# Kernel tuning notes

Hardware: AMD Instinct MI355X
Metric: run time of the kernel (lower is better)

Reference implementation:

```python
import jax, jax.numpy as jnp
import numpy as np
import math

B, N, D, H = 4, 2048, 1024, 16
DH = D // H  # dim per head
OUT = 1024

def setup_inputs() -> dict:
    key0 = jax.random.key(0)
    ks = jax.random.split(key0, 12)
    s = 1.0 / math.sqrt(D)
    return {
        "key": jax.random.normal(ks[0], (B, N, D), jnp.float32),
        "value": jax.random.normal(ks[1], (B, N, D), jnp.float32),
        "query": jax.random.normal(ks[2], (B, N, D), jnp.float32),
        "Wk": jax.random.normal(ks[3], (D, D), jnp.float32) * s,
        "bk": jax.random.normal(ks[4], (D,), jnp.float32) * 0.01,
        "Wv": jax.random.normal(ks[5], (D, D), jnp.float32) * s,
        "bv": jax.random.normal(ks[6], (D,), jnp.float32) * 0.01,
        "Wq": jax.random.normal(ks[7], (D, D), jnp.float32) * s,
        "bq": jax.random.normal(ks[8], (D,), jnp.float32) * 0.01,
        "Wo": jax.random.normal(ks[9], (D, OUT), jnp.float32) * s,
        "bo": jax.random.normal(ks[10], (OUT,), jnp.float32) * 0.01,
    }

def reference(key, value, query, Wk, bk, Wv, bv, Wq, bq, Wo, bo):
    scale = math.sqrt(DH)
    k = (key @ Wk + bk).reshape(B, N, H, DH).transpose(0, 2, 1, 3)    # [B,H,N,DH]
    v = (value @ Wv + bv).reshape(B, N, H, DH).transpose(0, 2, 1, 3)
    q = ((query @ Wq + bq) / scale).reshape(B, N, H, DH).transpose(0, 2, 1, 3)
    scores = jnp.einsum('bhqd,bhkd->bhqk', q, k).astype(jnp.float32)  # [B,H,N,N]
    attn = jax.nn.softmax(scores, axis=-1).astype(q.dtype)
    # dropout p=0.0 (eval / identity)
    ctx = jnp.einsum('bhqk,bhkd->bhqd', attn, v)                      # [B,H,N,DH]
    ctx = ctx.transpose(0, 2, 1, 3).reshape(B, N, D)
    out = ctx @ Wo + bo                                               # [B,N,OUT]
    return out
```

## Files before the change

kernel.cpp:

```cpp
#include <hip/hip_runtime.h>
#include <hip/hip_bf16.h>
#include <stdint.h>

#define BB 4
#define NN 2048
#define DD 1024
#define HH 16
#define DHH 64
#define MM (BB*NN)

typedef unsigned short u16;
typedef unsigned int u32;
typedef __bf16 bf16x8_t __attribute__((ext_vector_type(8)));
typedef float f32x4_t __attribute__((ext_vector_type(4)));
typedef float f32x16_t __attribute__((ext_vector_type(16)));

__device__ inline u16 f2b(float f) {
    __hip_bfloat16 h = __float2bfloat16(f);
    return *(u16*)&h;
}

__device__ inline u32 pack2(float lo, float hi) {
    __hip_bfloat162 h2 = __float22bfloat162_rn(make_float2(lo, hi));
    return *(u32*)&h2;
}

__device__ inline void gload16(const void* g, void* l) {
    __builtin_amdgcn_global_load_lds(
        (const __attribute__((address_space(1))) void*)g,
        (__attribute__((address_space(3))) void*)l, 16, 0, 0);
}

__global__ void cvt_kernel(const float* __restrict__ in, u16* __restrict__ out) {
    int i = (blockIdx.x * 256 + threadIdx.x) * 4;
    float4 v = *(const float4*)(in + i);
    ushort4 o;
    o.x = f2b(v.x); o.y = f2b(v.y); o.z = f2b(v.z); o.w = f2b(v.w);
    *(ushort4*)(out + i) = o;
}

__global__ void wtrans_kernel(const float* __restrict__ W0, const float* __restrict__ W1,
                              const float* __restrict__ W2, const float* __restrict__ W3,
                              u16* __restrict__ out_base) {
    int z = blockIdx.z;
    const float* W = (z == 0) ? W0 : (z == 1) ? W1 : (z == 2) ? W2 : W3;
    u16* o = out_base + (size_t)z * DD * DD;
    __shared__ float tile[64][65];
    int t = threadIdx.x;
    int r0 = t >> 6;
    int c = t & 63;
    int kb = blockIdx.x, nb = blockIdx.y;
#pragma unroll
    for (int i = 0; i < 16; ++i) {
        int r = i * 4 + r0;
        tile[r][c] = W[(size_t)(kb * 64 + r) * DD + nb * 64 + c];
    }
    __syncthreads();
#pragma unroll
    for (int i = 0; i < 16; ++i) {
        int r = i * 4 + r0;
        o[(size_t)(nb * 64 + r) * DD + kb * 64 + c] = f2b(tile[c][r]);
    }
}

__global__ void vtrans_kernel(const u16* __restrict__ in, u16* __restrict__ out) {
    __shared__ u16 tile[64][65];
    const int t = threadIdx.x;
    const int r0 = t >> 6;
    const int c = t & 63;
    const int nt = blockIdx.x;
    const int bh = blockIdx.y;
    const int b = bh >> 4, h = bh & 15;
    const u16* src = in + ((size_t)(b * 2048 + nt * 64)) * DD + h * 64;
#pragma unroll
    for (int i = 0; i < 16; ++i) {
        int r = i * 4 + r0;
        tile[r][c] = src[(size_t)r * DD + c];
    }
    __syncthreads();
    u16* dst = out + ((size_t)bh * 64) * NN + nt * 64;
#pragma unroll
    for (int i = 0; i < 16; ++i) {
        int r = i * 4 + r0;
        dst[(size_t)r * NN + c] = tile[c][r];
    }
}

template<int OUT_F32>
__global__ __launch_bounds__(256, 2)
void gemm_bt(const u16* __restrict__ A, const u16* __restrict__ Bt,
             const float* __restrict__ bias, void* __restrict__ Cout, float scale) {
    __shared__ u16 As[128 * 64];
    __shared__ u16 Bs[128 * 64];
    const int t = threadIdx.x;
    const int w = t >> 6, l = t & 63;
    const int wm = w >> 1, wn = w & 1;
    const int g = l >> 4, c = l & 15;
    const int bm = blockIdx.x, bn = blockIdx.y;

    const f32x4_t vzero = {0.f, 0.f, 0.f, 0.f};
    f32x4_t acc[4][4];
#pragma unroll
    for (int m = 0; m < 4; ++m)
#pragma unroll
        for (int n = 0; n < 4; ++n) acc[m][n] = vzero;

    const int srow = l >> 3;
    const int scol = ((l & 7) ^ srow) << 3;
    const int sa = (l & 7) << 4;

    for (int ks = 0; ks < 16; ++ks) {
#pragma unroll
        for (int i = 0; i < 4; ++i) {
            int chunk = w * 4 + i;
            int row = chunk * 8 + srow;
            const u16* ga = A + (size_t)(bm * 128 + row) * DD + ks * 64 + scol;
            gload16(ga, As + chunk * 512);
            const u16* gb = Bt + (size_t)(bn * 128 + row) * DD + ks * 64 + scol;
            gload16(gb, Bs + chunk * 512);
        }
        __syncthreads();

        bf16x8_t af[4][2], bfr[4][2];
#pragma unroll
        for (int m = 0; m < 4; ++m) {
            int rowa = wm * 64 + m * 16 + c;
#pragma unroll
            for (int kk = 0; kk < 2; ++kk)
                af[m][kk] = *(const bf16x8_t*)&As[rowa * 64 + (((kk * 64 + g * 16) ^ sa) >> 1)];
        }
#pragma unroll
        for (int n = 0; n < 4; ++n) {
            int rowb = wn * 64 + n * 16 + c;
#pragma unroll
            for (int kk = 0; kk < 2; ++kk)
                bfr[n][kk] = *(const bf16x8_t*)&Bs[rowb * 64 + (((kk * 64 + g * 16) ^ sa) >> 1)];
        }
#pragma unroll
        for (int kk = 0; kk < 2; ++kk)
#pragma unroll
            for (int m = 0; m < 4; ++m)
#pragma unroll
                for (int n = 0; n < 4; ++n)
                    acc[m][n] = __builtin_amdgcn_mfma_f32_16x16x32_bf16(
                        af[m][kk], bfr[n][kk], acc[m][n], 0, 0, 0);
        __syncthreads();
    }

#pragma unroll
    for (int n = 0; n < 4; ++n) {
        int col = bn * 128 + wn * 64 + n * 16 + c;
        float bv = bias[col];
#pragma unroll
        for (int m = 0; m < 4; ++m) {
            int row = bm * 128 + wm * 64 + m * 16 + g * 4;
#pragma unroll
            for (int j = 0; j < 4; ++j) {
                float v = (acc[m][n][j] + bv) * scale;
                if (OUT_F32)
                    ((float*)Cout)[(size_t)(row + j) * DD + col] = v;
                else
                    ((u16*)Cout)[(size_t)(row + j) * DD + col] = f2b(v);
            }
        }
    }
}

__global__ __launch_bounds__(256, 2)
void attn32_kernel(const u16* __restrict__ qb, const u16* __restrict__ kb,
                   const u16* __restrict__ vt, u16* __restrict__ ctx) {
    __shared__ u16 Kt[2][64 * 64];
    __shared__ u16 Vs[2][64 * 64];
    const int t = threadIdx.x;
    const int w = t >> 6, l = t & 63;
    const int hl = l >> 5, l31 = l & 31, l7 = l & 7, l3 = l >> 3;

    const int f = blockIdx.y * 8 + blockIdx.x;
    const int wg = (f & 7) * 64 + (f >> 3);
    const int qt = wg & 7, bh = wg >> 3;
    const int b = bh >> 4, h = bh & 15;
    const int hoff = h * DHH;
    const size_t kv0 = (size_t)b * NN;
    const size_t vt0 = (size_t)bh * DHH;

    const size_t qrow_base = (size_t)(b * NN + qt * 256 + w * 64);
    bf16x8_t qf[2][4];
#pragma unroll
    for (int qm = 0; qm < 2; ++qm)
#pragma unroll
        for (int dks = 0; dks < 4; ++dks)
            qf[qm][dks] = *(const bf16x8_t*)&qb[(qrow_base + qm * 32 + l31) * DD +
                                                hoff + dks * 16 + hl * 8];

    f32x16_t accO[2][2];
#pragma unroll
    for (int qm = 0; qm < 2; ++qm)
#pragma unroll
        for (int dt = 0; dt < 2; ++dt)
#pragma unroll
            for (int r = 0; r < 16; ++r) accO[qm][dt][r] = 0.f;
    float lacc[2] = {0.f, 0.f};

    const int scol2 = (l7 ^ l3) << 3;
    const u16* kp[2];
    const u16* vp[2];
#pragma unroll
    for (int i = 0; i < 2; ++i) {
        const int ch = w * 2 + i, r = ch * 8 + l3, rr = (r >> 2) & 3;
        const int pr = (rr == 1 || rr == 2) ? (r ^ 12) : r;
        kp[i] = kb + (kv0 + pr) * DD + hoff + scol2;
        vp[i] = vt + (vt0 + r) * NN + scol2;
    }

#define STAGE(buf_)                                                          \
    do {                                                                     \
        _Pragma("unroll")                                                    \
        for (int i_ = 0; i_ < 2; ++i_) {                                     \
            gload16(kp[i_], &Kt[buf_][(w * 2 + i_) * 512]);                  \
            gload16(vp[i_], &Vs[buf_][(w * 2 + i_) * 512]);                  \
        }                                                                    \
        _Pragma("unroll")                                                    \
        for (int i_ = 0; i_ < 2; ++i_) { kp[i_] += 64 * DD; vp[i_] += 64; }  \
    } while (0)

    STAGE(0);

    for (int kt = 0; kt < NN / 64; ++kt) {
        const int cur = kt & 1;
        if (kt < NN / 64 - 1) {
            STAGE(cur ^ 1);
            asm volatile("s_waitcnt vmcnt(4)" ::: "memory");
        } else {
            asm volatile("s_waitcnt vmcnt(0)" ::: "memory");
        }
        __builtin_amdgcn_s_barrier();
        asm volatile("" ::: "memory");

        const char* Kc = (const char*)Kt[cur];
        const char* Vc = (const char*)Vs[cur];

        bf16x8_t kf[2][4];
#pragma unroll
        for (int kt32 = 0; kt32 < 2; ++kt32)
#pragma unroll
            for (int dks = 0; dks < 4; ++dks)
                kf[kt32][dks] = *(const bf16x8_t*)(Kc + (kt32 * 32 + l31) * 128 +
                                                   ((dks * 32 + hl * 16) ^ (l7 << 4)));

        f32x16_t accS[2][2];
        __builtin_amdgcn_s_setprio(1);
#pragma unroll
        for (int qm = 0; qm < 2; ++qm)
#pragma unroll
            for (int kt32 = 0; kt32 < 2; ++kt32) {
#pragma unroll
                for (int r = 0; r < 16; ++r) accS[qm][kt32][r] = 0.f;
#pragma unroll
                for (int dks = 0; dks < 4; ++dks)
                    accS[qm][kt32] = __builtin_amdgcn_mfma_f32_32x32x16_bf16(
                        kf[kt32][dks], qf[qm][dks], accS[qm][kt32], 0, 0, 0);
            }
        __builtin_amdgcn_s_setprio(0);

#pragma unroll
        for (int qm = 0; qm < 2; ++qm) {
#pragma unroll
            for (int kt32 = 0; kt32 < 2; ++kt32)
#pragma unroll
                for (int r = 0; r < 16; ++r)
                    accS[qm][kt32][r] = __builtin_amdgcn_exp2f(accS[qm][kt32][r]);
            f32x16_t sv = accS[qm][0] + accS[qm][1];
            float s8[8];
#pragma unroll
            for (int r = 0; r < 8; ++r) s8[r] = sv[r] + sv[r + 8];
#pragma unroll
            for (int sl = 4; sl >= 1; sl >>= 1)
#pragma unroll
                for (int r = 0; r < sl; ++r) s8[r] += s8[r + sl];
            lacc[qm] += s8[0];
        }

        bf16x8_t vf[4][2];
#pragma unroll
        for (int pm = 0; pm < 4; ++pm)
#pragma unroll
            for (int dt = 0; dt < 2; ++dt)
                vf[pm][dt] = *(const bf16x8_t*)(Vc + (dt * 32 + l31) * 128 +
                                                ((pm * 32 + hl * 16) ^ (l7 << 4)));

        __builtin_amdgcn_s_setprio(1);
#pragma unroll
        for (int qm = 0; qm < 2; ++qm)
#pragma unroll
            for (int pm = 0; pm < 4; ++pm) {
                const int kt32 = pm >> 1, half = pm & 1;
                union { u32 u[4]; bf16x8_t v; } pu;
#pragma unroll
                for (int j2 = 0; j2 < 4; ++j2)
                    pu.u[j2] = pack2(accS[qm][kt32][half * 8 + 2 * j2],
                                     accS[qm][kt32][half * 8 + 2 * j2 + 1]);
#pragma unroll
                for (int dt = 0; dt < 2; ++dt)
                    accO[qm][dt] = __builtin_amdgcn_mfma_f32_32x32x16_bf16(
                        vf[pm][dt], pu.v, accO[qm][dt], 0, 0, 0);
            }
        __builtin_amdgcn_s_setprio(0);

        asm volatile("" ::: "memory");
        __builtin_amdgcn_s_barrier();
        asm volatile("" ::: "memory");
    }
#undef STAGE

#pragma unroll
    for (int qm = 0; qm < 2; ++qm) {
        float rsum = lacc[qm] + __shfl_xor(lacc[qm], 32);
        const float rl = 1.0f / rsum;
        const size_t qrow = qrow_base + qm * 32 + l31;
#pragma unroll
        for (int dt = 0; dt < 2; ++dt)
#pragma unroll
            for (int m = 0; m < 4; ++m) {
                ushort4 o;
                o.x = f2b(accO[qm][dt][4 * m + 0] * rl);
                o.y = f2b(accO[qm][dt][4 * m + 1] * rl);
                o.z = f2b(accO[qm][dt][4 * m + 2] * rl);
                o.w = f2b(accO[qm][dt][4 * m + 3] * rl);
                *(ushort4*)&ctx[qrow * DD + hoff + dt * 32 + m * 8 + hl * 4] = o;
            }
    }
}

extern "C" void kernel_launch(void* const* d_in, const int* in_sizes, int n_in,
                              void* d_out, int out_size, void* d_ws, size_t ws_size,
                              hipStream_t stream) {
    (void)in_sizes; (void)n_in; (void)out_size; (void)ws_size;
    const float* key   = (const float*)d_in[0];
    const float* value = (const float*)d_in[1];
    const float* query = (const float*)d_in[2];
    const float* Wk = (const float*)d_in[3];
    const float* bk = (const float*)d_in[4];
    const float* Wv = (const float*)d_in[5];
    const float* bv = (const float*)d_in[6];
    const float* Wq = (const float*)d_in[7];
    const float* bq = (const float*)d_in[8];
    const float* Wo = (const float*)d_in[9];
    const float* bo = (const float*)d_in[10];

    char* ws = (char*)d_ws;
    const size_t MB = 1024 * 1024;
    u16* qbuf = (u16*)(ws + 0 * MB);
    u16* kbuf = (u16*)(ws + 16 * MB);
    u16* vbuf = (u16*)(ws + 32 * MB);
    u16* WtK  = (u16*)(ws + 48 * MB);
    u16* WtV  = (u16*)(ws + 50 * MB);
    u16* WtQ  = (u16*)(ws + 52 * MB);
    u16* WtO  = (u16*)(ws + 54 * MB);
    u16* xb   = (u16*)(ws + 56 * MB);

    const int nelem = MM * DD;
    const int cvt_blocks = nelem / (256 * 4);

    wtrans_kernel<<<dim3(16, 16, 4), 256, 0, stream>>>(Wk, Wv, Wq, Wo, WtK);

    cvt_kernel<<<cvt_blocks, 256, 0, stream>>>(value, xb);
    gemm_bt<0><<<dim3(64, 8), 256, 0, stream>>>(xb, WtV, bv, vbuf, 1.0f);
    cvt_kernel<<<cvt_blocks, 256, 0, stream>>>(key, xb);
    gemm_bt<0><<<dim3(64, 8), 256, 0, stream>>>(xb, WtK, bk, kbuf, 1.0f);
    cvt_kernel<<<cvt_blocks, 256, 0, stream>>>(query, xb);
    gemm_bt<0><<<dim3(64, 8), 256, 0, stream>>>(xb, WtQ, bq, qbuf, 0.125f * 1.4426950408889634f);

    u16* VT = xb;
    vtrans_kernel<<<dim3(32, 64), 256, 0, stream>>>(vbuf, VT);

    u16* ctx = vbuf;
    attn32_kernel<<<dim3(8, 64), 256, 0, stream>>>(qbuf, kbuf, VT, ctx);

    gemm_bt<1><<<dim3(64, 8), 256, 0, stream>>>(ctx, WtO, bo, d_out, 1.0f);
}
```

Before: 211.0 us.

## Give each wave private K/V LDS tiles to drop block barriers

Each of the four waves now stages its own 32-key K and V tiles into a private double-buffered LDS region, so the per-iteration block-wide s_barrier calls are removed and waves advance independently. The key tile per iteration shrinks from 64 to 32, which doubles the iteration count, and V uses a new 64-byte-row swizzle. The row-sum reduction is deferred to the epilogue by keeping 8 partial sums per row. The cost is that each wave loads K/V itself, so global/L2 traffic for K/V rises fourfold per workgroup, and LDS grows from 32KB to 64KB per block, which may limit occupancy.

```diff
diff --git a/kernel.cpp b/kernel.cpp
--- a/kernel.cpp
+++ b/kernel.cpp
@@ -169,8 +169,8 @@
 __global__ __launch_bounds__(256, 2)
 void attn32_kernel(const u16* __restrict__ qb, const u16* __restrict__ kb,
                    const u16* __restrict__ vt, u16* __restrict__ ctx) {
-    __shared__ u16 Kt[2][64 * 64];
-    __shared__ u16 Vs[2][64 * 64];
+    __shared__ u16 KL[4][2][2048];
+    __shared__ u16 VL[4][2][2048];
     const int t = threadIdx.x;
     const int w = t >> 6, l = t & 63;
     const int hl = l >> 5, l31 = l & 31, l7 = l & 7, l3 = l >> 3;
@@ -199,122 +199,123 @@
         for (int dt = 0; dt < 2; ++dt)
 #pragma unroll
             for (int r = 0; r < 16; ++r) accO[qm][dt][r] = 0.f;
-    float lacc[2] = {0.f, 0.f};
-
-    const int scol2 = (l7 ^ l3) << 3;
-    const u16* kp[2];
-    const u16* vp[2];
-#pragma unroll
-    for (int i = 0; i < 2; ++i) {
-        const int ch = w * 2 + i, r = ch * 8 + l3, rr = (r >> 2) & 3;
+    float lacc8[2][8];
+#pragma unroll
+    for (int qm = 0; qm < 2; ++qm)
+#pragma unroll
+        for (int r = 0; r < 8; ++r) lacc8[qm][r] = 0.f;
+
+    const u16* kp[4];
+#pragma unroll
+    for (int i = 0; i < 4; ++i) {
+        const int r = i * 8 + l3, rr = (r >> 2) & 3;
         const int pr = (rr == 1 || rr == 2) ? (r ^ 12) : r;
-        kp[i] = kb + (kv0 + pr) * DD + hoff + scol2;
-        vp[i] = vt + (vt0 + r) * NN + scol2;
-    }
-
-#define STAGE(buf_)                                                          \
+        kp[i] = kb + (kv0 + pr) * DD + hoff + ((l7 ^ l3) << 3);
+    }
+    const u16* vp[4];
+#pragma unroll
+    for (int i = 0; i < 4; ++i) {
+        const int r4 = l >> 2;
+        vp[i] = vt + (vt0 + i * 16 + r4) * NN + (((l & 3) ^ (r4 & 3)) << 3);
+    }
+
+    u16* Kw0 = &KL[w][0][0];
+    u16* Vw0 = &VL[w][0][0];
+
+#define STAGE(S_)                                                            \
     do {                                                                     \
         _Pragma("unroll")                                                    \
-        for (int i_ = 0; i_ < 2; ++i_) {                                     \
-            gload16(kp[i_], &Kt[buf_][(w * 2 + i_) * 512]);                  \
-            gload16(vp[i_], &Vs[buf_][(w * 2 + i_) * 512]);                  \
+        for (int i_ = 0; i_ < 4; ++i_) {                                     \
+            gload16(kp[i_], Kw0 + (S_) * 2048 + i_ * 512);                   \
+            gload16(vp[i_], Vw0 + (S_) * 2048 + i_ * 512);                   \
         }                                                                    \
         _Pragma("unroll")                                                    \
-        for (int i_ = 0; i_ < 2; ++i_) { kp[i_] += 64 * DD; vp[i_] += 64; }  \
+        for (int i_ = 0; i_ < 4; ++i_) { kp[i_] += 32 * DD; vp[i_] += 32; }  \
     } while (0)
 
     STAGE(0);
 
-    for (int kt = 0; kt < NN / 64; ++kt) {
+#pragma unroll 1
+    for (int kt = 0; kt < NN / 32; ++kt) {
         const int cur = kt & 1;
-        if (kt < NN / 64 - 1) {
+        if (kt < NN / 32 - 1) {
             STAGE(cur ^ 1);
-            asm volatile("s_waitcnt vmcnt(4)" ::: "memory");
+            asm volatile("s_waitcnt vmcnt(8)" ::: "memory");
         } else {
             asm volatile("s_waitcnt vmcnt(0)" ::: "memory");
         }
-        __builtin_amdgcn_s_barrier();
-        asm volatile("" ::: "memory");
-
-        const char* Kc = (const char*)Kt[cur];
-        const char* Vc = (const char*)Vs[cur];
-
-        bf16x8_t kf[2][4];
-#pragma unroll
-        for (int kt32 = 0; kt32 < 2; ++kt32)
+
+        const char* Kc = (const char*)(Kw0 + cur * 2048);
+        const char* Vc = (const char*)(Vw0 + cur * 2048);
+
+        bf16x8_t kf[4];
+#pragma unroll
+        for (int dks = 0; dks < 4; ++dks)
+            kf[dks] = *(const bf16x8_t*)(Kc + l31 * 128 +
+                                         ((dks * 32 + hl * 16) ^ (l7 << 4)));
+
+        f32x16_t accS[2];
+        __builtin_amdgcn_s_setprio(1);
+#pragma unroll
+        for (int qm = 0; qm < 2; ++qm) {
+#pragma unroll
+            for (int r = 0; r < 16; ++r) accS[qm][r] = 0.f;
 #pragma unroll
             for (int dks = 0; dks < 4; ++dks)
-                kf[kt32][dks] = *(const bf16x8_t*)(Kc + (kt32 * 32 + l31) * 128 +
-                                                   ((dks * 32 + hl * 16) ^ (l7 << 4)));
-
-        f32x16_t accS[2][2];
+                accS[qm] = __builtin_amdgcn_mfma_f32_32x32x16_bf16(
+                    kf[dks], qf[qm][dks], accS[qm], 0, 0, 0);
+        }
+        __builtin_amdgcn_s_setprio(0);
+
+#pragma unroll
+        for (int qm = 0; qm < 2; ++qm) {
+#pragma unroll
+            for (int r = 0; r < 16; ++r)
+                accS[qm][r] = __builtin_amdgcn_exp2f(accS[qm][r]);
+#pragma unroll
+            for (int r = 0; r < 8; ++r)
+                lacc8[qm][r] += accS[qm][r] + accS[qm][r + 8];
+        }
+
+        bf16x8_t vf[2][2];
+#pragma unroll
+        for (int pm = 0; pm < 2; ++pm)
+#pragma unroll
+            for (int dt = 0; dt < 2; ++dt) {
+                const int row = dt * 32 + l31;
+                vf[pm][dt] = *(const bf16x8_t*)(Vc + row * 64 +
+                                                (((pm * 2 + hl) ^ (row & 3)) << 4));
+            }
+
         __builtin_amdgcn_s_setprio(1);
 #pragma unroll
         for (int qm = 0; qm < 2; ++qm)
 #pragma unroll
-            for (int kt32 = 0; kt32 < 2; ++kt32) {
-#pragma unroll
-                for (int r = 0; r < 16; ++r) accS[qm][kt32][r] = 0.f;
-#pragma unroll
-                for (int dks = 0; dks < 4; ++dks)
-                    accS[qm][kt32] = __builtin_amdgcn_mfma_f32_32x32x16_bf16(
-                        kf[kt32][dks], qf[qm][dks], accS[qm][kt32], 0, 0, 0);
-            }
-        __builtin_amdgcn_s_setprio(0);
-
-#pragma unroll
-        for (int qm = 0; qm < 2; ++qm) {
-#pragma unroll
-            for (int kt32 = 0; kt32 < 2; ++kt32)
-#pragma unroll
-                for (int r = 0; r < 16; ++r)
-                    accS[qm][kt32][r] = __builtin_amdgcn_exp2f(accS[qm][kt32][r]);
-            f32x16_t sv = accS[qm][0] + accS[qm][1];
-            float s8[8];
-#pragma unroll
-            for (int r = 0; r < 8; ++r) s8[r] = sv[r] + sv[r + 8];
-#pragma unroll
-            for (int sl = 4; sl >= 1; sl >>= 1)
-#pragma unroll
-                for (int r = 0; r < sl; ++r) s8[r] += s8[r + sl];
-            lacc[qm] += s8[0];
-        }
-
-        bf16x8_t vf[4][2];
-#pragma unroll
-        for (int pm = 0; pm < 4; ++pm)
-#pragma unroll
-            for (int dt = 0; dt < 2; ++dt)
-                vf[pm][dt] = *(const bf16x8_t*)(Vc + (dt * 32 + l31) * 128 +
-                                                ((pm * 32 + hl * 16) ^ (l7 << 4)));
-
-        __builtin_amdgcn_s_setprio(1);
-#pragma unroll
-        for (int qm = 0; qm < 2; ++qm)
-#pragma unroll
-            for (int pm = 0; pm < 4; ++pm) {
-                const int kt32 = pm >> 1, half = pm & 1;
+            for (int pm = 0; pm < 2; ++pm) {
                 union { u32 u[4]; bf16x8_t v; } pu;
 #pragma unroll
                 for (int j2 = 0; j2 < 4; ++j2)
-                    pu.u[j2] = pack2(accS[qm][kt32][half * 8 + 2 * j2],
-                                     accS[qm][kt32][half * 8 + 2 * j2 + 1]);
+                    pu.u[j2] = pack2(accS[qm][pm * 8 + 2 * j2],
+                                     accS[qm][pm * 8 + 2 * j2 + 1]);
 #pragma unroll
                 for (int dt = 0; dt < 2; ++dt)
                     accO[qm][dt] = __builtin_amdgcn_mfma_f32_32x32x16_bf16(
                         vf[pm][dt], pu.v, accO[qm][dt], 0, 0, 0);
             }
         __builtin_amdgcn_s_setprio(0);
-
-        asm volatile("" ::: "memory");
-        __builtin_amdgcn_s_barrier();
-        asm volatile("" ::: "memory");
     }
 #undef STAGE
 
 #pragma unroll
     for (int qm = 0; qm < 2; ++qm) {
-        float rsum = lacc[qm] + __shfl_xor(lacc[qm], 32);
+        float s8[8];
+#pragma unroll
+        for (int r = 0; r < 8; ++r) s8[r] = lacc8[qm][r];
+#pragma unroll
+        for (int sl = 4; sl >= 1; sl >>= 1)
+#pragma unroll
+            for (int r = 0; r < sl; ++r) s8[r] += s8[r + sl];
+        float rsum = s8[0] + __shfl_xor(s8[0], 32);
         const float rl = 1.0f / rsum;
         const size_t qrow = qrow_base + qm * 32 + l31;
 #pragma unroll
```

Result: slower. 219.2 us (+3.9%).
